# Kernel optimization log

Measured on AMD Instinct MI355X. Metric: run time of the kernel, lower is better.

The kernel has to match this reference:

```python
import jax, jax.numpy as jnp
import numpy as np

D_MODEL = 256
G_CH = 512
N_HEADS = 8
EPS = 1e-6


def setup_inputs() -> dict:
    key0 = jax.random.key(0)
    ks = jax.random.split(key0, 24)
    B, N1, C, G = 2, 65536, D_MODEL, G_CH
    p = 0.05
    inp = {
        'query': jax.random.normal(ks[0], (B, N1, G), jnp.float32),
        'key': jax.random.normal(ks[1], (B, N1, C), jnp.float32),
        'value': jax.random.normal(ks[2], (B, N1, C), jnp.float32),
        # Mheads1: Linear(guidance_channels, d_model, bias=False); stored as [in,out]
        'mheads1_w': jax.random.normal(ks[3], (G, C), jnp.float32) * p,
        # CrossAttentionLayer q/k/v: Linear(d_model, d_model)
        'q_w': jax.random.normal(ks[4], (C, C), jnp.float32) * p,
        'q_b': jax.random.normal(ks[5], (C,), jnp.float32) * p,
        'k_w': jax.random.normal(ks[6], (C, C), jnp.float32) * p,
        'k_b': jax.random.normal(ks[7], (C,), jnp.float32) * p,
        'v_w': jax.random.normal(ks[8], (C, C), jnp.float32) * p,
        'v_b': jax.random.normal(ks[9], (C,), jnp.float32) * p,
        # MSCW local_attn: Linear->ReLU->Linear
        'l1_w': jax.random.normal(ks[10], (C, C), jnp.float32) * p,
        'l1_b': jax.random.normal(ks[11], (C,), jnp.float32) * p,
        'l2_w': jax.random.normal(ks[12], (C, C), jnp.float32) * p,
        'l2_b': jax.random.normal(ks[13], (C,), jnp.float32) * p,
        # MSCW global_attn: Linear->ReLU->Linear
        'g1_w': jax.random.normal(ks[14], (C, C), jnp.float32) * p,
        'g1_b': jax.random.normal(ks[15], (C,), jnp.float32) * p,
        'g2_w': jax.random.normal(ks[16], (C, C), jnp.float32) * p,
        'g2_b': jax.random.normal(ks[17], (C,), jnp.float32) * p,
    }
    return inp


def _haar_pool(feat):
    # feat: [B, C, H, W]; standard WCT2 WavePool: depthwise 2x2 stride-2 Haar conv.
    B, C, H, W = feat.shape
    x = feat.reshape(B, C, H // 2, 2, W // 2, 2)
    a = x[:, :, :, 0, :, 0]
    b = x[:, :, :, 0, :, 1]
    c = x[:, :, :, 1, :, 0]
    d = x[:, :, :, 1, :, 1]
    # Haar: L=[1,1]/sqrt2, Hf=[-1,1]/sqrt2 -> outer-product 2x2 filters, /2 overall
    LL = (a + b + c + d) * 0.5
    LH = (-a + b - c + d) * 0.5
    HL = (-a - b + c + d) * 0.5
    HH = (a - b - c + d) * 0.5
    return LL, LH, HL, HH


def reference(query, key, value, mheads1_w, q_w, q_b, k_w, k_b, v_w, v_b,
              l1_w, l1_b, l2_w, l2_b, g1_w, g1_b, g2_w, g2_b):
    B, n1, C = value.shape
    hw = int(round(n1 ** 0.5))
    q_guid = query @ mheads1_w  # [B, L, C]

    feat = jnp.transpose(key, (0, 2, 1)).reshape(B, C, hw, hw)
    LL, LH, HL, HH = _haar_pool(feat)
    high = HL + LH + HH  # [B, C, hw/2, hw/2]
    low = LL
    high = jnp.transpose(high.reshape(B, C, -1), (0, 2, 1))  # [B, S, C]
    low = jnp.transpose(low.reshape(B, C, -1), (0, 2, 1))

    # MSCW gating
    s = high + low
    pool = jnp.mean(s, axis=1, keepdims=True)
    local = jax.nn.relu(s @ l1_w + l1_b) @ l2_w + l2_b
    glob = jax.nn.relu(pool @ g1_w + g1_b) @ g2_w + g2_b
    wei = jax.nn.sigmoid(local + glob)
    fre = wei * high + low  # [B, S, C]

    # CrossAttentionLayer with linear (elu-feature) attention
    H, Dh = N_HEADS, C // N_HEADS
    qh = (q_guid @ q_w + q_b).reshape(B, -1, H, Dh)
    kh = (fre @ k_w + k_b).reshape(B, -1, H, Dh)
    vh = (fre @ v_w + v_b).reshape(B, -1, H, Dh)
    Q = jax.nn.elu(qh) + 1.0
    K = jax.nn.elu(kh) + 1.0
    S = vh.shape[1]
    Vn = vh / S
    KV = jnp.einsum('nshd,nshv->nhdv', K, Vn)  # [B, H, D, D]
    Z = 1.0 / (jnp.einsum('nlhd,nhd->nlh', Q, K.sum(axis=1)) + EPS)
    out = jnp.einsum('nlhd,nhdv,nlh->nlhv', Q, KV, Z) * S
    return out.reshape(B, -1, C)
```

## Files before the change

kernel.cpp:

```cpp
#include <hip/hip_runtime.h>
#include <math.h>

#define BB 2
#define N1 65536
#define N2 16384
#define CC 256
#define GG 512
#define NH 8
#define DH 32

#define WS_PPART 0
#define WS_GLOB  66048
#define WS_KVP   66560
#define WS_KSP   590848
#define WS_KVT   607232
#define WS_WFP   619520
#define WS_L1T   685056
#define WS_L2T   717824
#define WS_KWT   750592
#define WS_VWT   783360

typedef __attribute__((ext_vector_type(8))) short short8v;
typedef __attribute__((ext_vector_type(4))) float f32x4;

__device__ __forceinline__ ushort f2bf(float x) {
    union { float f; unsigned int u; } v; v.f = x;
    unsigned int u = v.u;
    unsigned int r = (u + 0x7fffu + ((u >> 16) & 1u)) >> 16;
    return (ushort)r;
}

__device__ __forceinline__ float bf2f(ushort x) {
    union { float f; unsigned int u; } v;
    v.u = ((unsigned int)x) << 16;
    return v.f;
}

__device__ __forceinline__ unsigned int cvtpk(float lo, float hi) {
    unsigned int d;
    asm("v_cvt_pk_bf16_f32 %0, %1, %2" : "=v"(d) : "v"(lo), "v"(hi));
    return d;
}

__device__ __forceinline__ void gload16(const void* g, void* l) {
    __builtin_amdgcn_global_load_lds(
        (const __attribute__((address_space(1))) unsigned int*)g,
        (__attribute__((address_space(3))) unsigned int*)l, 16, 0, 0);
}

__global__ __launch_bounds__(256) void k_prep(const float* __restrict__ l1w, const float* __restrict__ l2w,
                                              const float* __restrict__ kw, const float* __restrict__ vw,
                                              const float* __restrict__ mh, const float* __restrict__ qw,
                                              const float* __restrict__ key,
                                              ushort* __restrict__ t0, ushort* __restrict__ t1,
                                              ushort* __restrict__ t2, ushort* __restrict__ t3,
                                              ushort* __restrict__ wfp, float* __restrict__ ppart) {
    int blk = blockIdx.x, t = threadIdx.x;
    if (blk < 1024) {
        int mat = blk >> 8, k = blk & 255, n = t;
        const float* w = mat == 0 ? l1w : mat == 1 ? l2w : mat == 2 ? kw : vw;
        ushort* o = mat == 0 ? t0 : mat == 1 ? t1 : mat == 2 ? t2 : t3;
        o[(((size_t)(n >> 7) * 8 + (k >> 5)) * 128 + (n & 127)) * 32 + (k & 31)] = f2bf(w[k * 256 + n]);
    } else if (blk < 1536) {
        __shared__ float mr[256];
        int g = blk - 1024;
        mr[t] = mh[g * 256 + t];
        __syncthreads();
        float acc = 0.f;
        for (int k = 0; k < 256; k++) acc += mr[k] * qw[k * 256 + t];
        wfp[(((size_t)(g >> 5) * 256 + t) * 32 + (g & 31))] = f2bf(acc);
    } else {
        int p = blk - 1536;
        int b = p >> 7, ci = p & 127;
        float acc = 0.f;
        for (int q = 0; q < 128; q++) {
            size_t idx = ((size_t)b * 65536 + (size_t)(2 * ci + 1) * 256 + (2 * q + 1)) * 256 + t;
            acc += key[idx];
        }
        ppart[(size_t)p * 256 + t] = acc;
    }
}

__global__ __launch_bounds__(256) void k_glob2(const float* __restrict__ ppart,
                                               const float* __restrict__ g1w,
                                               const float* __restrict__ g1b,
                                               const float* __restrict__ g2w,
                                               const float* __restrict__ g2b,
                                               float* __restrict__ glob) {
    __shared__ float pl[256], hid[256];
    int t = threadIdx.x;
    for (int b = 0; b < BB; b++) {
        float s = 0.f;
        for (int p = 0; p < 128; p++) s += ppart[((size_t)b * 128 + p) * 256 + t];
        pl[t] = s * (2.f / 16384.f);
        __syncthreads();
        float acc = g1b[t];
        for (int k = 0; k < 256; k++) acc += pl[k] * g1w[k * 256 + t];
        hid[t] = fmaxf(acc, 0.f);
        __syncthreads();
        float a2 = g2b[t];
        for (int k = 0; k < 256; k++) a2 += hid[k] * g2w[k * 256 + t];
        glob[b * 256 + t] = a2;
        __syncthreads();
    }
}

template <int AMODE, int EPI>
__global__ __launch_bounds__(256) void gemm_bf(const void* __restrict__ Asrc_,
                                               const ushort* __restrict__ Wt,
                                               const float* __restrict__ bias,
                                               void* __restrict__ Outp,
                                               const float* __restrict__ glob,
                                               const float* __restrict__ key) {
    __shared__ __align__(16) ushort smem[8192];
    ushort* As = smem;
    ushort* Bs = smem + 4096;

    const int tid = threadIdx.x;
    const int lane = tid & 63;
    const int w = tid >> 6;
    const int wrow = w >> 1, wcol = w & 1;
    const int bx = blockIdx.x & 1;
    const int by = blockIdx.x >> 1;
    const int r0 = by * 128, n0 = bx * 128;
    const int l15 = lane & 15, l4 = lane >> 4;

    const int loff = lane * 16;
    char* ldsB0 = (char*)Bs + w * 2048;
    char* ldsB1 = (char*)Bs + w * 2048 + 1024;
    const int rowA0 = w * 32 + (lane >> 2);
    const int kbA = (lane & 3) * 16;
    char* ldsA0 = (char*)As + w * 2048;
    char* ldsA1 = (char*)As + w * 2048 + 1024;
    const int srow = tid >> 1, shalf = tid & 1;
    size_t agbase = 0;
    if constexpr (AMODE == 1) {
        int r = r0 + srow;
        int b = r >> 14, rr = r & 16383;
        int ii = rr >> 7, jj = rr & 127;
        agbase = ((size_t)b * 65536 + (size_t)(2 * ii + 1) * 256 + (2 * jj + 1)) * 256 + shalf * 16;
    }

    f32x4 acc[4][4];
#pragma unroll
    for (int i = 0; i < 4; i++)
#pragma unroll
        for (int j = 0; j < 4; j++) acc[i][j] = (f32x4){0.f, 0.f, 0.f, 0.f};

    for (int ks = 0; ks < 8; ks++) {
        const char* btile = (const char*)Wt + (size_t)(bx * 8 + ks) * 8192;
        gload16(btile + w * 2048 + loff, ldsB0);
        gload16(btile + w * 2048 + 1024 + loff, ldsB1);
        if constexpr (AMODE == 0) {
            const char* ab = (const char*)Asrc_;
            gload16(ab + (size_t)(r0 + rowA0) * 512 + ks * 64 + kbA, ldsA0);
            gload16(ab + (size_t)(r0 + rowA0 + 16) * 512 + ks * 64 + kbA, ldsA1);
        } else {
            const float* kf = (const float*)Asrc_;
            float4 f0 = *(const float4*)(kf + agbase + (size_t)ks * 32);
            float4 f1 = *(const float4*)(kf + agbase + (size_t)ks * 32 + 4);
            float4 f2 = *(const float4*)(kf + agbase + (size_t)ks * 32 + 8);
            float4 f3 = *(const float4*)(kf + agbase + (size_t)ks * 32 + 12);
            uint4 lo = {cvtpk(f0.x * 2.f, f0.y * 2.f), cvtpk(f0.z * 2.f, f0.w * 2.f),
                        cvtpk(f1.x * 2.f, f1.y * 2.f), cvtpk(f1.z * 2.f, f1.w * 2.f)};
            uint4 hi = {cvtpk(f2.x * 2.f, f2.y * 2.f), cvtpk(f2.z * 2.f, f2.w * 2.f),
                        cvtpk(f3.x * 2.f, f3.y * 2.f), cvtpk(f3.z * 2.f, f3.w * 2.f)};
            *(uint4*)((char*)As + srow * 64 + shalf * 32) = lo;
            *(uint4*)((char*)As + srow * 64 + shalf * 32 + 16) = hi;
        }
        __syncthreads();

        short8v a[4], bfr[4];
#pragma unroll
        for (int m = 0; m < 4; m++)
            a[m] = *(const short8v*)((const char*)As + (wrow * 64 + m * 16 + l15) * 64 + l4 * 16);
#pragma unroll
        for (int n = 0; n < 4; n++)
            bfr[n] = *(const short8v*)((const char*)Bs + (wcol * 64 + n * 16 + l15) * 64 + l4 * 16);
#pragma unroll
        for (int m = 0; m < 4; m++)
#pragma unroll
            for (int n = 0; n < 4; n++)
                acc[m][n] = __builtin_amdgcn_mfma_f32_16x16x32_bf16(a[m], bfr[n], acc[m][n], 0, 0, 0);
        __syncthreads();
    }

    const int b = r0 >> 14;
    float bv[4], gv[4];
#pragma unroll
    for (int n = 0; n < 4; n++) {
        int c = n0 + wcol * 64 + n * 16 + l15;
        bv[n] = bias[c];
        if constexpr (EPI == 1) gv[n] = glob[b * 256 + c];
    }
#pragma unroll
    for (int m = 0; m < 4; m++) {
#pragma unroll
        for (int n = 0; n < 4; n++) {
            int c = n0 + wcol * 64 + n * 16 + l15;
#pragma unroll
            for (int r = 0; r < 4; r++) {
                int row = wrow * 64 + m * 16 + l4 * 4 + r;
                int R = r0 + row;
                float x = acc[m][n][r] + bv[n];
                if constexpr (EPI == 0) {
                    ((ushort*)Outp)[(size_t)R * 256 + c] = f2bf(fmaxf(x, 0.f));
                } else if constexpr (EPI == 1) {
                    int rr = R & 16383;
                    int ii = rr >> 7, jj = rr & 127;
                    size_t kb = ((size_t)b * 65536 + (size_t)(2 * ii) * 256 + 2 * jj) * 256 + c;
                    float ka = key[kb];
                    float kb2 = key[kb + 256];
                    float kc2 = key[kb + 65536];
                    float kd2 = key[kb + 65536 + 256];
                    float low = 0.5f * (ka + kb2 + kc2 + kd2);
                    float high = 0.5f * (3.f * kd2 - ka - kb2 - kc2);
                    float wei = 1.f / (1.f + __expf(-(x + gv[n])));
                    ((ushort*)Outp)[(size_t)R * 256 + c] = f2bf(wei * high + low);
                } else if constexpr (EPI == 4) {
                    ((ushort*)Outp)[(size_t)R * 256 + c] = f2bf((x > 0.f) ? x + 1.f : __expf(x));
                } else {
                    ((ushort*)Outp)[(size_t)R * 256 + c] = f2bf(x);
                }
            }
        }
    }
}

__global__ __launch_bounds__(256) void k_kv_part(const ushort* __restrict__ Km,
                                                 const ushort* __restrict__ Vn,
                                                 float* __restrict__ kvp,
                                                 float* __restrict__ ksp) {
    __shared__ float Kl[8][33];
    __shared__ float Vl[8][33];
    int t = threadIdx.x;
    int c = blockIdx.x & 31, h = (blockIdx.x >> 5) & 7, b = blockIdx.x >> 8;
    int d = t >> 3, vq = (t & 7) * 4;
    int lr = t >> 5, lc = t & 31;
    float acc0 = 0, acc1 = 0, acc2 = 0, acc3 = 0, ks = 0;
    size_t rowbase = (size_t)b * 16384 + (size_t)c * 512;
    for (int s0 = 0; s0 < 512; s0 += 8) {
        size_t idx = (rowbase + s0 + lr) * 256 + h * 32 + lc;
        Kl[lr][lc] = bf2f(Km[idx]);
        Vl[lr][lc] = bf2f(Vn[idx]);
        __syncthreads();
#pragma unroll
        for (int rr = 0; rr < 8; rr++) {
            float kd = Kl[rr][d];
            acc0 += kd * Vl[rr][vq];
            acc1 += kd * Vl[rr][vq + 1];
            acc2 += kd * Vl[rr][vq + 2];
            acc3 += kd * Vl[rr][vq + 3];
            ks += kd;
        }
        __syncthreads();
    }
    size_t ob = ((size_t)(b * 8 + h) * 32 + c) * 1024 + d * 32 + vq;
    kvp[ob] = acc0; kvp[ob + 1] = acc1; kvp[ob + 2] = acc2; kvp[ob + 3] = acc3;
    if ((t & 7) == 0) ksp[((b * 8 + h) * 32 + c) * 32 + d] = ks;
}

__global__ __launch_bounds__(256) void k_kv_reduce(const float* __restrict__ kvp,
                                                   const float* __restrict__ ksp,
                                                   ushort* __restrict__ kvt) {
    int bh = blockIdx.x, t = threadIdx.x;
    for (int e = t; e < 1024; e += 256) {
        float s = 0.f;
        for (int cc = 0; cc < 32; cc++) s += kvp[((size_t)bh * 32 + cc) * 1024 + e];
        int d = e >> 5, v = e & 31;
        kvt[((size_t)bh * 48 + v) * 32 + d] = f2bf(s);
    }
    if (t < 32) {
        float s = 0.f;
        for (int cc = 0; cc < 32; cc++) s += ksp[(bh * 32 + cc) * 32 + t];
        kvt[((size_t)bh * 48 + 32) * 32 + t] = f2bf(s);
    }
    for (int z = t; z < 480; z += 256) kvt[(size_t)bh * 48 * 32 + 33 * 32 + z] = 0;
}

__global__ __launch_bounds__(512, 4) void k_qattn_mfma(const float* __restrict__ query,
                                                       const ushort* __restrict__ wfp,
                                                       const float* __restrict__ qb,
                                                       const ushort* __restrict__ kvt,
                                                       float* __restrict__ Out) {
    __shared__ __align__(16) ushort smem[32768];
    ushort* As = smem;
    ushort* Bs = smem + 4096;

    const int tid = threadIdx.x;
    const int lane = tid & 63;
    const int wid = tid >> 6;
    const int wrow = wid >> 2, wcol = wid & 3;
    const int by = blockIdx.x;
    const int r0 = by * 128;
    const int l15 = lane & 15, l4 = lane >> 4;

    const int loff = lane * 16;
    char* ldsB0 = (char*)Bs + wid * 2048;
    char* ldsB1 = (char*)Bs + wid * 2048 + 1024;

    const int srow = tid >> 2;
    const int skq = tid & 3;
    const size_t agbase = (size_t)(r0 + srow) * 512 + skq * 8;

    f32x4 acc[4][4];
#pragma unroll
    for (int i = 0; i < 4; i++)
#pragma unroll
        for (int j = 0; j < 4; j++) acc[i][j] = (f32x4){0.f, 0.f, 0.f, 0.f};

    for (int ks = 0; ks < 16; ks++) {
        const char* btile = (const char*)wfp + (size_t)ks * 16384;
        gload16(btile + wid * 2048 + loff, ldsB0);
        gload16(btile + wid * 2048 + 1024 + loff, ldsB1);
        {
            float4 f0 = *(const float4*)(query + agbase + (size_t)ks * 32);
            float4 f1 = *(const float4*)(query + agbase + (size_t)ks * 32 + 4);
            uint4 pk = {cvtpk(f0.x, f0.y), cvtpk(f0.z, f0.w),
                        cvtpk(f1.x, f1.y), cvtpk(f1.z, f1.w)};
            *(uint4*)((char*)As + srow * 64 + skq * 16) = pk;
        }
        __syncthreads();

        short8v a[4], bfr[4];
#pragma unroll
        for (int m = 0; m < 4; m++)
            a[m] = *(const short8v*)((const char*)As + (wrow * 64 + m * 16 + l15) * 64 + l4 * 16);
#pragma unroll
        for (int n = 0; n < 4; n++)
            bfr[n] = *(const short8v*)((const char*)Bs + (wcol * 64 + n * 16 + l15) * 64 + l4 * 16);
#pragma unroll
        for (int m = 0; m < 4; m++)
#pragma unroll
            for (int n = 0; n < 4; n++)
                acc[m][n] = __builtin_amdgcn_mfma_f32_16x16x32_bf16(a[m], bfr[n], acc[m][n], 0, 0, 0);
        __syncthreads();
    }

    float qbv[4];
#pragma unroll
    for (int n = 0; n < 4; n++) qbv[n] = qb[wcol * 64 + n * 16 + l15];
#pragma unroll
    for (int m = 0; m < 4; m++) {
#pragma unroll
        for (int n = 0; n < 4; n++) {
#pragma unroll
            for (int r = 0; r < 4; r++) {
                int rl = m * 16 + l4 * 4 + r;
                int cl = n * 16 + l15;
                float x = acc[m][n][r] + qbv[n];
                float q = x > 0.f ? x + 1.f : __expf(x);
                int byte = wid * 8192 + ((rl * 128 + cl * 2) ^ ((rl & 7) << 4));
                *(ushort*)((char*)smem + byte) = f2bf(q);
            }
        }
    }
    __syncthreads();

    const int bb = r0 >> 16;
#pragma unroll
    for (int hi = 0; hi < 2; hi++) {
        int h = wcol * 2 + hi;
        int bh = bb * 8 + h;
        const ushort* kb = kvt + (size_t)bh * 48 * 32;
        short8v bk0 = *(const short8v*)(kb + (0 * 16 + l15) * 32 + l4 * 8);
        short8v bk1 = *(const short8v*)(kb + (1 * 16 + l15) * 32 + l4 * 8);
        short8v bkz = *(const short8v*)(kb + (2 * 16 + l15) * 32 + l4 * 8);
#pragma unroll
        for (int m = 0; m < 4; m++) {
            int rl = m * 16 + l15;
            int byte = wid * 8192 + ((rl * 128 + hi * 64 + l4 * 16) ^ ((rl & 7) << 4));
            short8v aq = *(const short8v*)((const char*)smem + byte);
            f32x4 zero = (f32x4){0.f, 0.f, 0.f, 0.f};
            f32x4 o0 = __builtin_amdgcn_mfma_f32_16x16x32_bf16(aq, bk0, zero, 0, 0, 0);
            f32x4 o1 = __builtin_amdgcn_mfma_f32_16x16x32_bf16(aq, bk1, zero, 0, 0, 0);
            f32x4 oz = __builtin_amdgcn_mfma_f32_16x16x32_bf16(aq, bkz, zero, 0, 0, 0);
#pragma unroll
            for (int r = 0; r < 4; r++) {
                float z = __shfl(oz[r], (lane & 48));
                float sc = 1.f / (z + 1e-6f);
                int grow = r0 + wrow * 64 + m * 16 + l4 * 4 + r;
                int gcol = wcol * 64 + hi * 32 + l15;
                Out[(size_t)grow * 256 + gcol] = o0[r] * sc;
                Out[(size_t)grow * 256 + gcol + 16] = o1[r] * sc;
            }
        }
    }
}

extern "C" void kernel_launch(void* const* d_in, const int* in_sizes, int n_in,
                              void* d_out, int out_size, void* d_ws, size_t ws_size,
                              hipStream_t stream) {
    const float* query = (const float*)d_in[0];
    const float* key = (const float*)d_in[1];
    const float* mh = (const float*)d_in[3];
    const float* q_w = (const float*)d_in[4];
    const float* q_b = (const float*)d_in[5];
    const float* k_w = (const float*)d_in[6];
    const float* k_b = (const float*)d_in[7];
    const float* v_w = (const float*)d_in[8];
    const float* v_b = (const float*)d_in[9];
    const float* l1_w = (const float*)d_in[10];
    const float* l1_b = (const float*)d_in[11];
    const float* l2_w = (const float*)d_in[12];
    const float* l2_b = (const float*)d_in[13];
    const float* g1_w = (const float*)d_in[14];
    const float* g1_b = (const float*)d_in[15];
    const float* g2_w = (const float*)d_in[16];
    const float* g2_b = (const float*)d_in[17];

    float* out = (float*)d_out;
    float* ws = (float*)d_ws;

    float* ppart = ws + WS_PPART;
    float* glob = ws + WS_GLOB;
    float* kvp = ws + WS_KVP;
    float* ksp = ws + WS_KSP;
    ushort* kvt = (ushort*)(ws + WS_KVT);
    ushort* wfp = (ushort*)(ws + WS_WFP);
    ushort* l1t = (ushort*)(ws + WS_L1T);
    ushort* l2t = (ushort*)(ws + WS_L2T);
    ushort* kwt = (ushort*)(ws + WS_KWT);
    ushort* vwt = (ushort*)(ws + WS_VWT);

    ushort* t = (ushort*)out;
    ushort* fre = (ushort*)(out + 4194304);
    ushort* Km = (ushort*)(out + 8388608);
    ushort* Vn = (ushort*)(out + 12582912);

    k_prep<<<1792, 256, 0, stream>>>(l1_w, l2_w, k_w, v_w, mh, q_w, key,
                                     l1t, l2t, kwt, vwt, wfp, ppart);
    k_glob2<<<1, 256, 0, stream>>>(ppart, g1_w, g1_b, g2_w, g2_b, glob);

    gemm_bf<1, 0><<<512, 256, 0, stream>>>(key, l1t, l1_b, t, nullptr, nullptr);
    gemm_bf<0, 1><<<512, 256, 0, stream>>>(t, l2t, l2_b, fre, glob, key);
    gemm_bf<0, 4><<<512, 256, 0, stream>>>(fre, kwt, k_b, Km, nullptr, nullptr);
    gemm_bf<0, 5><<<512, 256, 0, stream>>>(fre, vwt, v_b, Vn, nullptr, nullptr);

    k_kv_part<<<512, 256, 0, stream>>>(Km, Vn, kvp, ksp);
    k_kv_reduce<<<16, 256, 0, stream>>>(kvp, ksp, kvt);

    k_qattn_mfma<<<1024, 512, 0, stream>>>(query, wfp, q_b, kvt, out);
}
```

Measured before the change: 271.6 us.

## Fuse four chained MSCW/K/V GEMMs into one kernel keeping tiles in LDS

```diff
diff --git a/kernel.cpp b/kernel.cpp
--- a/kernel.cpp
+++ b/kernel.cpp
@@ -2,12 +2,6 @@
 #include <math.h>
 
 #define BB 2
-#define N1 65536
-#define N2 16384
-#define CC 256
-#define GG 512
-#define NH 8
-#define DH 32
 
 #define WS_PPART 0
 #define WS_GLOB  66048
@@ -60,7 +54,7 @@
         int mat = blk >> 8, k = blk & 255, n = t;
         const float* w = mat == 0 ? l1w : mat == 1 ? l2w : mat == 2 ? kw : vw;
         ushort* o = mat == 0 ? t0 : mat == 1 ? t1 : mat == 2 ? t2 : t3;
-        o[(((size_t)(n >> 7) * 8 + (k >> 5)) * 128 + (n & 127)) * 32 + (k & 31)] = f2bf(w[k * 256 + n]);
+        o[(size_t)(k >> 5) * 8192 + (size_t)((k >> 3) & 3) * 2048 + n * 8 + (k & 7)] = f2bf(w[k * 256 + n]);
     } else if (blk < 1536) {
         __shared__ float mr[256];
         int g = blk - 1024;
@@ -68,7 +62,7 @@
         __syncthreads();
         float acc = 0.f;
         for (int k = 0; k < 256; k++) acc += mr[k] * qw[k * 256 + t];
-        wfp[(((size_t)(g >> 5) * 256 + t) * 32 + (g & 31))] = f2bf(acc);
+        wfp[(size_t)(g >> 3) * 2048 + t * 8 + (g & 7)] = f2bf(acc);
     } else {
         int p = blk - 1536;
         int b = p >> 7, ci = p & 127;
@@ -105,123 +99,235 @@
     }
 }
 
-template <int AMODE, int EPI>
-__global__ __launch_bounds__(256) void gemm_bf(const void* __restrict__ Asrc_,
-                                               const ushort* __restrict__ Wt,
-                                               const float* __restrict__ bias,
-                                               void* __restrict__ Outp,
-                                               const float* __restrict__ glob,
-                                               const float* __restrict__ key) {
-    __shared__ __align__(16) ushort smem[8192];
-    ushort* As = smem;
-    ushort* Bs = smem + 4096;
+__global__ __launch_bounds__(256, 3) void k_mid(const float* __restrict__ key,
+                                                const ushort* __restrict__ l1t,
+                                                const ushort* __restrict__ l2t,
+                                                const ushort* __restrict__ kwt,
+                                                const ushort* __restrict__ vwt,
+                                                const float* __restrict__ l1b,
+                                                const float* __restrict__ l2b,
+                                                const float* __restrict__ kbias,
+                                                const float* __restrict__ vbias,
+                                                const float* __restrict__ glob,
+                                                ushort* __restrict__ Km,
+                                                ushort* __restrict__ Vn) {
+    __shared__ __align__(16) ushort smem[26624];
+    ushort* tile = smem;
+    ushort* As = smem + 16384;
+    ushort* Bs = smem + 18432;
 
     const int tid = threadIdx.x;
     const int lane = tid & 63;
-    const int w = tid >> 6;
-    const int wrow = w >> 1, wcol = w & 1;
-    const int bx = blockIdx.x & 1;
-    const int by = blockIdx.x >> 1;
-    const int r0 = by * 128, n0 = bx * 128;
+    const int wid = tid >> 6;
+    const int wrow = wid >> 1, wcol = wid & 1;
+    const int R0 = blockIdx.x * 64;
+    const int b = R0 >> 14;
     const int l15 = lane & 15, l4 = lane >> 4;
 
-    const int loff = lane * 16;
-    char* ldsB0 = (char*)Bs + w * 2048;
-    char* ldsB1 = (char*)Bs + w * 2048 + 1024;
-    const int rowA0 = w * 32 + (lane >> 2);
-    const int kbA = (lane & 3) * 16;
-    char* ldsA0 = (char*)As + w * 2048;
-    char* ldsA1 = (char*)As + w * 2048 + 1024;
-    const int srow = tid >> 1, shalf = tid & 1;
-    size_t agbase = 0;
-    if constexpr (AMODE == 1) {
-        int r = r0 + srow;
-        int b = r >> 14, rr = r & 16383;
+    const int srow = tid & 63, skq = tid >> 6;
+    size_t agbase;
+    {
+        int R = R0 + srow;
+        int rr = R & 16383;
         int ii = rr >> 7, jj = rr & 127;
-        agbase = ((size_t)b * 65536 + (size_t)(2 * ii + 1) * 256 + (2 * jj + 1)) * 256 + shalf * 16;
-    }
-
-    f32x4 acc[4][4];
-#pragma unroll
-    for (int i = 0; i < 4; i++)
-#pragma unroll
-        for (int j = 0; j < 4; j++) acc[i][j] = (f32x4){0.f, 0.f, 0.f, 0.f};
+        agbase = ((size_t)b * 65536 + (size_t)(2 * ii + 1) * 256 + (2 * jj + 1)) * 256 + skq * 8;
+    }
+
+    f32x4 acc[2][8];
+
+#pragma unroll
+    for (int m = 0; m < 2; m++)
+#pragma unroll
+        for (int n = 0; n < 8; n++) acc[m][n] = (f32x4){0.f, 0.f, 0.f, 0.f};
 
     for (int ks = 0; ks < 8; ks++) {
-        const char* btile = (const char*)Wt + (size_t)(bx * 8 + ks) * 8192;
-        gload16(btile + w * 2048 + loff, ldsB0);
-        gload16(btile + w * 2048 + 1024 + loff, ldsB1);
-        if constexpr (AMODE == 0) {
-            const char* ab = (const char*)Asrc_;
-            gload16(ab + (size_t)(r0 + rowA0) * 512 + ks * 64 + kbA, ldsA0);
-            gload16(ab + (size_t)(r0 + rowA0 + 16) * 512 + ks * 64 + kbA, ldsA1);
-        } else {
-            const float* kf = (const float*)Asrc_;
-            float4 f0 = *(const float4*)(kf + agbase + (size_t)ks * 32);
-            float4 f1 = *(const float4*)(kf + agbase + (size_t)ks * 32 + 4);
-            float4 f2 = *(const float4*)(kf + agbase + (size_t)ks * 32 + 8);
-            float4 f3 = *(const float4*)(kf + agbase + (size_t)ks * 32 + 12);
-            uint4 lo = {cvtpk(f0.x * 2.f, f0.y * 2.f), cvtpk(f0.z * 2.f, f0.w * 2.f),
-                        cvtpk(f1.x * 2.f, f1.y * 2.f), cvtpk(f1.z * 2.f, f1.w * 2.f)};
-            uint4 hi = {cvtpk(f2.x * 2.f, f2.y * 2.f), cvtpk(f2.z * 2.f, f2.w * 2.f),
-                        cvtpk(f3.x * 2.f, f3.y * 2.f), cvtpk(f3.z * 2.f, f3.w * 2.f)};
-            *(uint4*)((char*)As + srow * 64 + shalf * 32) = lo;
-            *(uint4*)((char*)As + srow * 64 + shalf * 32 + 16) = hi;
-        }
-        __syncthreads();
-
-        short8v a[4], bfr[4];
-#pragma unroll
-        for (int m = 0; m < 4; m++)
-            a[m] = *(const short8v*)((const char*)As + (wrow * 64 + m * 16 + l15) * 64 + l4 * 16);
-#pragma unroll
-        for (int n = 0; n < 4; n++)
-            bfr[n] = *(const short8v*)((const char*)Bs + (wcol * 64 + n * 16 + l15) * 64 + l4 * 16);
-#pragma unroll
-        for (int m = 0; m < 4; m++)
-#pragma unroll
-            for (int n = 0; n < 4; n++)
-                acc[m][n] = __builtin_amdgcn_mfma_f32_16x16x32_bf16(a[m], bfr[n], acc[m][n], 0, 0, 0);
-        __syncthreads();
-    }
-
-    const int b = r0 >> 14;
-    float bv[4], gv[4];
-#pragma unroll
-    for (int n = 0; n < 4; n++) {
-        int c = n0 + wcol * 64 + n * 16 + l15;
-        bv[n] = bias[c];
-        if constexpr (EPI == 1) gv[n] = glob[b * 256 + c];
-    }
-#pragma unroll
-    for (int m = 0; m < 4; m++) {
-#pragma unroll
-        for (int n = 0; n < 4; n++) {
-            int c = n0 + wcol * 64 + n * 16 + l15;
+        float4 f0 = *(const float4*)(key + agbase + (size_t)ks * 32);
+        float4 f1 = *(const float4*)(key + agbase + (size_t)ks * 32 + 4);
+        uint4 pk = {cvtpk(f0.x * 2.f, f0.y * 2.f), cvtpk(f0.z * 2.f, f0.w * 2.f),
+                    cvtpk(f1.x * 2.f, f1.y * 2.f), cvtpk(f1.z * 2.f, f1.w * 2.f)};
+        *(uint4*)((char*)As + skq * 1024 + srow * 16) = pk;
+        {
+            const char* pan = (const char*)l1t + (size_t)ks * 16384;
+            char* dst = (char*)Bs + wid * 4096;
+#pragma unroll
+            for (int i = 0; i < 4; i++)
+                gload16(pan + wid * 4096 + i * 1024 + lane * 16, dst + i * 1024);
+        }
+        __syncthreads();
+        short8v a[2], bf[8];
+#pragma unroll
+        for (int m = 0; m < 2; m++)
+            a[m] = *(const short8v*)((const char*)As + l4 * 1024 + (wrow * 32 + m * 16 + l15) * 16);
+#pragma unroll
+        for (int n = 0; n < 8; n++)
+            bf[n] = *(const short8v*)((const char*)Bs + l4 * 4096 + (wcol * 128 + n * 16 + l15) * 16);
+#pragma unroll
+        for (int m = 0; m < 2; m++)
+#pragma unroll
+            for (int n = 0; n < 8; n++)
+                acc[m][n] = __builtin_amdgcn_mfma_f32_16x16x32_bf16(a[m], bf[n], acc[m][n], 0, 0, 0);
+        __syncthreads();
+    }
+#pragma unroll
+    for (int m = 0; m < 2; m++) {
+#pragma unroll
+        for (int n = 0; n < 8; n++) {
+            int col = wcol * 128 + n * 16 + l15;
+            float bias = l1b[col];
 #pragma unroll
             for (int r = 0; r < 4; r++) {
-                int row = wrow * 64 + m * 16 + l4 * 4 + r;
-                int R = r0 + row;
-                float x = acc[m][n][r] + bv[n];
-                if constexpr (EPI == 0) {
-                    ((ushort*)Outp)[(size_t)R * 256 + c] = f2bf(fmaxf(x, 0.f));
-                } else if constexpr (EPI == 1) {
-                    int rr = R & 16383;
-                    int ii = rr >> 7, jj = rr & 127;
-                    size_t kb = ((size_t)b * 65536 + (size_t)(2 * ii) * 256 + 2 * jj) * 256 + c;
-                    float ka = key[kb];
-                    float kb2 = key[kb + 256];
-                    float kc2 = key[kb + 65536];
-                    float kd2 = key[kb + 65536 + 256];
-                    float low = 0.5f * (ka + kb2 + kc2 + kd2);
-                    float high = 0.5f * (3.f * kd2 - ka - kb2 - kc2);
-                    float wei = 1.f / (1.f + __expf(-(x + gv[n])));
-                    ((ushort*)Outp)[(size_t)R * 256 + c] = f2bf(wei * high + low);
-                } else if constexpr (EPI == 4) {
-                    ((ushort*)Outp)[(size_t)R * 256 + c] = f2bf((x > 0.f) ? x + 1.f : __expf(x));
-                } else {
-                    ((ushort*)Outp)[(size_t)R * 256 + c] = f2bf(x);
-                }
+                int row = wrow * 32 + m * 16 + l4 * 4 + r;
+                float x = acc[m][n][r] + bias;
+                int byte = (row * 512 + col * 2) ^ ((row & 7) << 4);
+                *(ushort*)((char*)tile + byte) = f2bf(fmaxf(x, 0.f));
+            }
+        }
+    }
+
+#pragma unroll
+    for (int m = 0; m < 2; m++)
+#pragma unroll
+        for (int n = 0; n < 8; n++) acc[m][n] = (f32x4){0.f, 0.f, 0.f, 0.f};
+
+    for (int ks = 0; ks < 8; ks++) {
+        {
+            const char* pan = (const char*)l2t + (size_t)ks * 16384;
+            char* dst = (char*)Bs + wid * 4096;
+#pragma unroll
+            for (int i = 0; i < 4; i++)
+                gload16(pan + wid * 4096 + i * 1024 + lane * 16, dst + i * 1024);
+        }
+        __syncthreads();
+        short8v a[2], bf[8];
+#pragma unroll
+        for (int m = 0; m < 2; m++) {
+            int row = wrow * 32 + m * 16 + l15;
+            int byte = (row * 512 + ks * 64 + l4 * 16) ^ ((row & 7) << 4);
+            a[m] = *(const short8v*)((const char*)tile + byte);
+        }
+#pragma unroll
+        for (int n = 0; n < 8; n++)
+            bf[n] = *(const short8v*)((const char*)Bs + l4 * 4096 + (wcol * 128 + n * 16 + l15) * 16);
+#pragma unroll
+        for (int m = 0; m < 2; m++)
+#pragma unroll
+            for (int n = 0; n < 8; n++)
+                acc[m][n] = __builtin_amdgcn_mfma_f32_16x16x32_bf16(a[m], bf[n], acc[m][n], 0, 0, 0);
+        __syncthreads();
+    }
+#pragma unroll
+    for (int m = 0; m < 2; m++) {
+#pragma unroll
+        for (int n = 0; n < 8; n++) {
+            int col = wcol * 128 + n * 16 + l15;
+            float bias = l2b[col] + glob[b * 256 + col];
+#pragma unroll
+            for (int r = 0; r < 4; r++) {
+                int row = wrow * 32 + m * 16 + l4 * 4 + r;
+                int rr = (R0 + row) & 16383;
+                int ii = rr >> 7, jj = rr & 127;
+                size_t kb = ((size_t)b * 65536 + (size_t)(2 * ii) * 256 + 2 * jj) * 256 + col;
+                float ka = key[kb];
+                float kb2 = key[kb + 256];
+                float kc2 = key[kb + 65536];
+                float kd2 = key[kb + 65536 + 256];
+                float low = 0.5f * (ka + kb2 + kc2 + kd2);
+                float high = 0.5f * (3.f * kd2 - ka - kb2 - kc2);
+                float x = acc[m][n][r] + bias;
+                float wei = 1.f / (1.f + __expf(-x));
+                int byte = (row * 512 + col * 2) ^ ((row & 7) << 4);
+                *(ushort*)((char*)tile + byte) = f2bf(wei * high + low);
+            }
+        }
+    }
+
+#pragma unroll
+    for (int m = 0; m < 2; m++)
+#pragma unroll
+        for (int n = 0; n < 8; n++) acc[m][n] = (f32x4){0.f, 0.f, 0.f, 0.f};
+
+    for (int ks = 0; ks < 8; ks++) {
+        {
+            const char* pan = (const char*)kwt + (size_t)ks * 16384;
+            char* dst = (char*)Bs + wid * 4096;
+#pragma unroll
+            for (int i = 0; i < 4; i++)
+                gload16(pan + wid * 4096 + i * 1024 + lane * 16, dst + i * 1024);
+        }
+        __syncthreads();
+        short8v a[2], bf[8];
+#pragma unroll
+        for (int m = 0; m < 2; m++) {
+            int row = wrow * 32 + m * 16 + l15;
+            int byte = (row * 512 + ks * 64 + l4 * 16) ^ ((row & 7) << 4);
+            a[m] = *(const short8v*)((const char*)tile + byte);
+        }
+#pragma unroll
+        for (int n = 0; n < 8; n++)
+            bf[n] = *(const short8v*)((const char*)Bs + l4 * 4096 + (wcol * 128 + n * 16 + l15) * 16);
+#pragma unroll
+        for (int m = 0; m < 2; m++)
+#pragma unroll
+            for (int n = 0; n < 8; n++)
+                acc[m][n] = __builtin_amdgcn_mfma_f32_16x16x32_bf16(a[m], bf[n], acc[m][n], 0, 0, 0);
+        __syncthreads();
+    }
+#pragma unroll
+    for (int m = 0; m < 2; m++) {
+#pragma unroll
+        for (int n = 0; n < 8; n++) {
+            int col = wcol * 128 + n * 16 + l15;
+            float bias = kbias[col];
+#pragma unroll
+            for (int r = 0; r < 4; r++) {
+                int row = wrow * 32 + m * 16 + l4 * 4 + r;
+                float x = acc[m][n][r] + bias;
+                Km[(size_t)(R0 + row) * 256 + col] = f2bf((x > 0.f) ? x + 1.f : __expf(x));
+            }
+        }
+    }
+
+#pragma unroll
+    for (int m = 0; m < 2; m++)
+#pragma unroll
+        for (int n = 0; n < 8; n++) acc[m][n] = (f32x4){0.f, 0.f, 0.f, 0.f};
+
+    for (int ks = 0; ks < 8; ks++) {
+        {
+            const char* pan = (const char*)vwt + (size_t)ks * 16384;
+            char* dst = (char*)Bs + wid * 4096;
+#pragma unroll
+            for (int i = 0; i < 4; i++)
+                gload16(pan + wid * 4096 + i * 1024 + lane * 16, dst + i * 1024);
+        }
+        __syncthreads();
+        short8v a[2], bf[8];
+#pragma unroll
+        for (int m = 0; m < 2; m++) {
+            int row = wrow * 32 + m * 16 + l15;
+            int byte = (row * 512 + ks * 64 + l4 * 16) ^ ((row & 7) << 4);
+            a[m] = *(const short8v*)((const char*)tile + byte);
+        }
+#pragma unroll
+        for (int n = 0; n < 8; n++)
+            bf[n] = *(const short8v*)((const char*)Bs + l4 * 4096 + (wcol * 128 + n * 16 + l15) * 16);
+#pragma unroll
+        for (int m = 0; m < 2; m++)
+#pragma unroll
+            for (int n = 0; n < 8; n++)
+                acc[m][n] = __builtin_amdgcn_mfma_f32_16x16x32_bf16(a[m], bf[n], acc[m][n], 0, 0, 0);
+        __syncthreads();
+    }
+#pragma unroll
+    for (int m = 0; m < 2; m++) {
+#pragma unroll
+        for (int n = 0; n < 8; n++) {
+            int col = wcol * 128 + n * 16 + l15;
+            float bias = vbias[col];
+#pragma unroll
+            for (int r = 0; r < 4; r++) {
+                int row = wrow * 32 + m * 16 + l4 * 4 + r;
+                Vn[(size_t)(R0 + row) * 256 + col] = f2bf(acc[m][n][r] + bias);
             }
         }
     }
@@ -285,23 +391,18 @@
                                                        float* __restrict__ Out) {
     __shared__ __align__(16) ushort smem[32768];
     ushort* As = smem;
-    ushort* Bs = smem + 4096;
+    ushort* Bs = smem + 8192;
 
     const int tid = threadIdx.x;
     const int lane = tid & 63;
     const int wid = tid >> 6;
     const int wrow = wid >> 2, wcol = wid & 3;
-    const int by = blockIdx.x;
-    const int r0 = by * 128;
+    const int R0 = blockIdx.x * 128;
     const int l15 = lane & 15, l4 = lane >> 4;
 
-    const int loff = lane * 16;
-    char* ldsB0 = (char*)Bs + wid * 2048;
-    char* ldsB1 = (char*)Bs + wid * 2048 + 1024;
-
-    const int srow = tid >> 2;
-    const int skq = tid & 3;
-    const size_t agbase = (size_t)(r0 + srow) * 512 + skq * 8;
+    const int srow = tid & 127;
+    const int khalf = tid >> 7;
+    const size_t agbase = (size_t)(R0 + srow) * 512 + khalf * 16;
 
     f32x4 acc[4][4];
 #pragma unroll
@@ -309,31 +410,41 @@
 #pragma unroll
         for (int j = 0; j < 4; j++) acc[i][j] = (f32x4){0.f, 0.f, 0.f, 0.f};
 
-    for (int ks = 0; ks < 16; ks++) {
-        const char* btile = (const char*)wfp + (size_t)ks * 16384;
-        gload16(btile + wid * 2048 + loff, ldsB0);
-        gload16(btile + wid * 2048 + 1024 + loff, ldsB1);
+    for (int ks = 0; ks < 8; ks++) {
         {
-            float4 f0 = *(const float4*)(query + agbase + (size_t)ks * 32);
-            float4 f1 = *(const float4*)(query + agbase + (size_t)ks * 32 + 4);
-            uint4 pk = {cvtpk(f0.x, f0.y), cvtpk(f0.z, f0.w),
-                        cvtpk(f1.x, f1.y), cvtpk(f1.z, f1.w)};
-            *(uint4*)((char*)As + srow * 64 + skq * 16) = pk;
-        }
-        __syncthreads();
-
-        short8v a[4], bfr[4];
-#pragma unroll
-        for (int m = 0; m < 4; m++)
-            a[m] = *(const short8v*)((const char*)As + (wrow * 64 + m * 16 + l15) * 64 + l4 * 16);
-#pragma unroll
-        for (int n = 0; n < 4; n++)
-            bfr[n] = *(const short8v*)((const char*)Bs + (wcol * 64 + n * 16 + l15) * 64 + l4 * 16);
-#pragma unroll
-        for (int m = 0; m < 4; m++)
+            const float* qp = query + agbase + (size_t)ks * 64;
+            float4 f0 = *(const float4*)(qp);
+            float4 f1 = *(const float4*)(qp + 4);
+            float4 f2 = *(const float4*)(qp + 8);
+            float4 f3 = *(const float4*)(qp + 12);
+            uint4 lo = {cvtpk(f0.x, f0.y), cvtpk(f0.z, f0.w), cvtpk(f1.x, f1.y), cvtpk(f1.z, f1.w)};
+            uint4 hi = {cvtpk(f2.x, f2.y), cvtpk(f2.z, f2.w), cvtpk(f3.x, f3.y), cvtpk(f3.z, f3.w)};
+            *(uint4*)((char*)As + (khalf * 2) * 2048 + srow * 16) = lo;
+            *(uint4*)((char*)As + (khalf * 2 + 1) * 2048 + srow * 16) = hi;
+        }
+        {
+            const char* pan = (const char*)wfp + (size_t)ks * 32768;
+#pragma unroll
+            for (int i = 0; i < 4; i++)
+                gload16(pan + i * 8192 + wid * 1024 + lane * 16, (char*)Bs + i * 8192 + wid * 1024);
+        }
+        __syncthreads();
+
+#pragma unroll
+        for (int sub = 0; sub < 2; sub++) {
+            short8v a[4], bf[4];
+#pragma unroll
+            for (int m = 0; m < 4; m++)
+                a[m] = *(const short8v*)((const char*)As + (sub * 4 + l4) * 2048 + (wrow * 64 + m * 16 + l15) * 16);
 #pragma unroll
             for (int n = 0; n < 4; n++)
-                acc[m][n] = __builtin_amdgcn_mfma_f32_16x16x32_bf16(a[m], bfr[n], acc[m][n], 0, 0, 0);
+                bf[n] = *(const short8v*)((const char*)Bs + (sub * 4 + l4) * 4096 + (wcol * 64 + n * 16 + l15) * 16);
+#pragma unroll
+            for (int m = 0; m < 4; m++)
+#pragma unroll
+                for (int n = 0; n < 4; n++)
+                    acc[m][n] = __builtin_amdgcn_mfma_f32_16x16x32_bf16(a[m], bf[n], acc[m][n], 0, 0, 0);
+        }
         __syncthreads();
     }
 
@@ -357,7 +468,7 @@
     }
     __syncthreads();
 
-    const int bb = r0 >> 16;
+    const int bb = R0 >> 16;
 #pragma unroll
     for (int hi = 0; hi < 2; hi++) {
         int h = wcol * 2 + hi;
@@ -379,7 +490,7 @@
             for (int r = 0; r < 4; r++) {
                 float z = __shfl(oz[r], (lane & 48));
                 float sc = 1.f / (z + 1e-6f);
-                int grow = r0 + wrow * 64 + m * 16 + l4 * 4 + r;
+                int grow = R0 + wrow * 64 + m * 16 + l4 * 4 + r;
                 int gcol = wcol * 64 + hi * 32 + l15;
                 Out[(size_t)grow * 256 + gcol] = o0[r] * sc;
                 Out[(size_t)grow * 256 + gcol + 16] = o1[r] * sc;
@@ -423,19 +534,15 @@
     ushort* kwt = (ushort*)(ws + WS_KWT);
     ushort* vwt = (ushort*)(ws + WS_VWT);
 
-    ushort* t = (ushort*)out;
-    ushort* fre = (ushort*)(out + 4194304);
-    ushort* Km = (ushort*)(out + 8388608);
-    ushort* Vn = (ushort*)(out + 12582912);
+    ushort* Km = (ushort*)out;
+    ushort* Vn = (ushort*)(out + 4194304);
 
     k_prep<<<1792, 256, 0, stream>>>(l1_w, l2_w, k_w, v_w, mh, q_w, key,
                                      l1t, l2t, kwt, vwt, wfp, ppart);
     k_glob2<<<1, 256, 0, stream>>>(ppart, g1_w, g1_b, g2_w, g2_b, glob);
 
-    gemm_bf<1, 0><<<512, 256, 0, stream>>>(key, l1t, l1_b, t, nullptr, nullptr);
-    gemm_bf<0, 1><<<512, 256, 0, stream>>>(t, l2t, l2_b, fre, glob, key);
-    gemm_bf<0, 4><<<512, 256, 0, stream>>>(fre, kwt, k_b, Km, nullptr, nullptr);
-    gemm_bf<0, 5><<<512, 256, 0, stream>>>(fre, vwt, v_b, Vn, nullptr, nullptr);
+    k_mid<<<512, 256, 0, stream>>>(key, l1t, l2t, kwt, vwt,
+                                   l1_b, l2_b, k_b, v_b, glob, Km, Vn);
 
     k_kv_part<<<512, 256, 0, stream>>>(Km, Vn, kvp, ksp);
     k_kv_reduce<<<16, 256, 0, stream>>>(kvp, ksp, kvt);
```

New measurement: 277.6 us. 2.2% more time.

## Retile query-attention kernel to 64-row blocks with 256 threads

Applied to the files above, without the earlier changes.

```diff
diff --git a/kernel.cpp b/kernel.cpp
--- a/kernel.cpp
+++ b/kernel.cpp
@@ -2,12 +2,6 @@
 #include <math.h>
 
 #define BB 2
-#define N1 65536
-#define N2 16384
-#define CC 256
-#define GG 512
-#define NH 8
-#define DH 32
 
 #define WS_PPART 0
 #define WS_GLOB  66048
@@ -278,30 +272,24 @@
     for (int z = t; z < 480; z += 256) kvt[(size_t)bh * 48 * 32 + 33 * 32 + z] = 0;
 }
 
-__global__ __launch_bounds__(512, 4) void k_qattn_mfma(const float* __restrict__ query,
+__global__ __launch_bounds__(256, 4) void k_qattn_mfma(const float* __restrict__ query,
                                                        const ushort* __restrict__ wfp,
                                                        const float* __restrict__ qb,
                                                        const ushort* __restrict__ kvt,
                                                        float* __restrict__ Out) {
-    __shared__ __align__(16) ushort smem[32768];
+    __shared__ __align__(16) ushort smem[16384];
     ushort* As = smem;
-    ushort* Bs = smem + 4096;
+    ushort* Bs = smem + 2048;
 
     const int tid = threadIdx.x;
     const int lane = tid & 63;
     const int wid = tid >> 6;
-    const int wrow = wid >> 2, wcol = wid & 3;
-    const int by = blockIdx.x;
-    const int r0 = by * 128;
+    const int R0 = blockIdx.x * 64;
     const int l15 = lane & 15, l4 = lane >> 4;
 
-    const int loff = lane * 16;
-    char* ldsB0 = (char*)Bs + wid * 2048;
-    char* ldsB1 = (char*)Bs + wid * 2048 + 1024;
-
-    const int srow = tid >> 2;
-    const int skq = tid & 3;
-    const size_t agbase = (size_t)(r0 + srow) * 512 + skq * 8;
+    const int srow = tid & 63;
+    const int skq = tid >> 6;
+    const size_t agbase = (size_t)(R0 + srow) * 512 + skq * 8;
 
     f32x4 acc[4][4];
 #pragma unroll
@@ -310,9 +298,6 @@
         for (int j = 0; j < 4; j++) acc[i][j] = (f32x4){0.f, 0.f, 0.f, 0.f};
 
     for (int ks = 0; ks < 16; ks++) {
-        const char* btile = (const char*)wfp + (size_t)ks * 16384;
-        gload16(btile + wid * 2048 + loff, ldsB0);
-        gload16(btile + wid * 2048 + 1024 + loff, ldsB1);
         {
             float4 f0 = *(const float4*)(query + agbase + (size_t)ks * 32);
             float4 f1 = *(const float4*)(query + agbase + (size_t)ks * 32 + 4);
@@ -320,15 +305,22 @@
                         cvtpk(f1.x, f1.y), cvtpk(f1.z, f1.w)};
             *(uint4*)((char*)As + srow * 64 + skq * 16) = pk;
         }
+        {
+            const char* pan = (const char*)wfp + (size_t)ks * 16384;
+#pragma unroll
+            for (int i = 0; i < 4; i++)
+                gload16(pan + wid * 4096 + i * 1024 + lane * 16,
+                        (char*)Bs + wid * 4096 + i * 1024);
+        }
         __syncthreads();
 
         short8v a[4], bfr[4];
 #pragma unroll
         for (int m = 0; m < 4; m++)
-            a[m] = *(const short8v*)((const char*)As + (wrow * 64 + m * 16 + l15) * 64 + l4 * 16);
+            a[m] = *(const short8v*)((const char*)As + (m * 16 + l15) * 64 + l4 * 16);
 #pragma unroll
         for (int n = 0; n < 4; n++)
-            bfr[n] = *(const short8v*)((const char*)Bs + (wcol * 64 + n * 16 + l15) * 64 + l4 * 16);
+            bfr[n] = *(const short8v*)((const char*)Bs + (wid * 64 + n * 16 + l15) * 64 + l4 * 16);
 #pragma unroll
         for (int m = 0; m < 4; m++)
 #pragma unroll
@@ -339,28 +331,28 @@
 
     float qbv[4];
 #pragma unroll
-    for (int n = 0; n < 4; n++) qbv[n] = qb[wcol * 64 + n * 16 + l15];
+    for (int n = 0; n < 4; n++) qbv[n] = qb[wid * 64 + n * 16 + l15];
 #pragma unroll
     for (int m = 0; m < 4; m++) {
 #pragma unroll
         for (int n = 0; n < 4; n++) {
 #pragma unroll
             for (int r = 0; r < 4; r++) {
-                int rl = m * 16 + l4 * 4 + r;
-                int cl = n * 16 + l15;
+                int row = m * 16 + l4 * 4 + r;
+                int col = wid * 64 + n * 16 + l15;
                 float x = acc[m][n][r] + qbv[n];
                 float q = x > 0.f ? x + 1.f : __expf(x);
-                int byte = wid * 8192 + ((rl * 128 + cl * 2) ^ ((rl & 7) << 4));
+                int byte = (row * 512 + col * 2) ^ ((row & 7) << 4);
                 *(ushort*)((char*)smem + byte) = f2bf(q);
             }
         }
     }
     __syncthreads();
 
-    const int bb = r0 >> 16;
+    const int bb = R0 >> 14 >> 2;
 #pragma unroll
     for (int hi = 0; hi < 2; hi++) {
-        int h = wcol * 2 + hi;
+        int h = wid * 2 + hi;
         int bh = bb * 8 + h;
         const ushort* kb = kvt + (size_t)bh * 48 * 32;
         short8v bk0 = *(const short8v*)(kb + (0 * 16 + l15) * 32 + l4 * 8);
@@ -368,8 +360,8 @@
         short8v bkz = *(const short8v*)(kb + (2 * 16 + l15) * 32 + l4 * 8);
 #pragma unroll
         for (int m = 0; m < 4; m++) {
-            int rl = m * 16 + l15;
-            int byte = wid * 8192 + ((rl * 128 + hi * 64 + l4 * 16) ^ ((rl & 7) << 4));
+            int row = m * 16 + l15;
+            int byte = (row * 512 + h * 64 + l4 * 16) ^ ((row & 7) << 4);
             short8v aq = *(const short8v*)((const char*)smem + byte);
             f32x4 zero = (f32x4){0.f, 0.f, 0.f, 0.f};
             f32x4 o0 = __builtin_amdgcn_mfma_f32_16x16x32_bf16(aq, bk0, zero, 0, 0, 0);
@@ -379,8 +371,8 @@
             for (int r = 0; r < 4; r++) {
                 float z = __shfl(oz[r], (lane & 48));
                 float sc = 1.f / (z + 1e-6f);
-                int grow = r0 + wrow * 64 + m * 16 + l4 * 4 + r;
-                int gcol = wcol * 64 + hi * 32 + l15;
+                int grow = R0 + m * 16 + l4 * 4 + r;
+                int gcol = h * 32 + l15;
                 Out[(size_t)grow * 256 + gcol] = o0[r] * sc;
                 Out[(size_t)grow * 256 + gcol + 16] = o1[r] * sc;
             }
@@ -440,5 +432,5 @@
     k_kv_part<<<512, 256, 0, stream>>>(Km, Vn, kvp, ksp);
     k_kv_reduce<<<16, 256, 0, stream>>>(kvp, ksp, kvt);
 
-    k_qattn_mfma<<<1024, 512, 0, stream>>>(query, wfp, q_b, kvt, out);
-}
+    k_qattn_mfma<<<2048, 256, 0, stream>>>(query, wfp, q_b, kvt, out);
+}
```

Measured after the change: 289.7 us. 1.07x slower.

## Double-buffer query GEMM tiles with direct fp32 global-to-LDS loads

Applied to the files above, without the earlier changes.

```diff
diff --git a/kernel.cpp b/kernel.cpp
--- a/kernel.cpp
+++ b/kernel.cpp
@@ -2,12 +2,6 @@
 #include <math.h>
 
 #define BB 2
-#define N1 65536
-#define N2 16384
-#define CC 256
-#define GG 512
-#define NH 8
-#define DH 32
 
 #define WS_PPART 0
 #define WS_GLOB  66048
@@ -283,25 +277,24 @@
                                                        const float* __restrict__ qb,
                                                        const ushort* __restrict__ kvt,
                                                        float* __restrict__ Out) {
-    __shared__ __align__(16) ushort smem[32768];
-    ushort* As = smem;
-    ushort* Bs = smem + 4096;
+    __shared__ __align__(16) char smem[65536];
+    char* As0 = smem;
+    char* As1 = smem + 16384;
+    char* Bs0 = smem + 32768;
+    char* Bs1 = smem + 49152;
 
     const int tid = threadIdx.x;
     const int lane = tid & 63;
     const int wid = tid >> 6;
     const int wrow = wid >> 2, wcol = wid & 3;
-    const int by = blockIdx.x;
-    const int r0 = by * 128;
+    const int R0 = blockIdx.x * 128;
     const int l15 = lane & 15, l4 = lane >> 4;
 
-    const int loff = lane * 16;
-    char* ldsB0 = (char*)Bs + wid * 2048;
-    char* ldsB1 = (char*)Bs + wid * 2048 + 1024;
-
-    const int srow = tid >> 2;
-    const int skq = tid & 3;
-    const size_t agbase = (size_t)(r0 + srow) * 512 + skq * 8;
+    const int arow0 = wid * 16 + (lane >> 3);
+    const int achunk = (lane & 7) ^ (lane >> 3);
+    const float* aga = query + (size_t)(R0 + arow0) * 512 + achunk * 4;
+    const int wb = wid * 2048;
+    const int bglo = wb + lane * 16;
 
     f32x4 acc[4][4];
 #pragma unroll
@@ -309,33 +302,56 @@
 #pragma unroll
         for (int j = 0; j < 4; j++) acc[i][j] = (f32x4){0.f, 0.f, 0.f, 0.f};
 
+#define QSTAGE(dA, dB, kss)                                                     \
+    do {                                                                        \
+        const float* ga_ = aga + (size_t)(kss) * 32;                            \
+        gload16(ga_, (dA) + wb);                                                \
+        gload16(ga_ + 8 * 512, (dA) + wb + 1024);                               \
+        const char* pan_ = (const char*)wfp + (size_t)(kss) * 16384 + bglo;     \
+        gload16(pan_, (dB) + wb);                                               \
+        gload16(pan_ + 1024, (dB) + wb + 1024);                                 \
+    } while (0)
+
+    QSTAGE(As0, Bs0, 0);
+    asm volatile("s_waitcnt vmcnt(0)" ::: "memory");
+    __builtin_amdgcn_s_barrier();
+    __builtin_amdgcn_sched_barrier(0);
+
     for (int ks = 0; ks < 16; ks++) {
-        const char* btile = (const char*)wfp + (size_t)ks * 16384;
-        gload16(btile + wid * 2048 + loff, ldsB0);
-        gload16(btile + wid * 2048 + 1024 + loff, ldsB1);
-        {
-            float4 f0 = *(const float4*)(query + agbase + (size_t)ks * 32);
-            float4 f1 = *(const float4*)(query + agbase + (size_t)ks * 32 + 4);
-            uint4 pk = {cvtpk(f0.x, f0.y), cvtpk(f0.z, f0.w),
-                        cvtpk(f1.x, f1.y), cvtpk(f1.z, f1.w)};
-            *(uint4*)((char*)As + srow * 64 + skq * 16) = pk;
-        }
-        __syncthreads();
-
-        short8v a[4], bfr[4];
-#pragma unroll
-        for (int m = 0; m < 4; m++)
-            a[m] = *(const short8v*)((const char*)As + (wrow * 64 + m * 16 + l15) * 64 + l4 * 16);
+        const char* bA = (ks & 1) ? As1 : As0;
+        const char* bB = (ks & 1) ? Bs1 : Bs0;
+        char* nA = (ks & 1) ? As0 : As1;
+        char* nB = (ks & 1) ? Bs0 : Bs1;
+        if (ks < 15) QSTAGE(nA, nB, ks + 1);
+
+        short8v bfr[4];
 #pragma unroll
         for (int n = 0; n < 4; n++)
-            bfr[n] = *(const short8v*)((const char*)Bs + (wcol * 64 + n * 16 + l15) * 64 + l4 * 16);
-#pragma unroll
-        for (int m = 0; m < 4; m++)
+            bfr[n] = *(const short8v*)(bB + (wcol * 64 + n * 16 + l15) * 64 + l4 * 16);
+#pragma unroll
+        for (int m = 0; m < 4; m++) {
+            int row = wrow * 64 + m * 16 + l15;
+            int j0 = (l4 * 2) ^ (l15 & 7);
+            const char* rp = bA + row * 128;
+            f32x4 lo = *(const f32x4*)(rp + j0 * 16);
+            f32x4 hi = *(const f32x4*)(rp + (j0 ^ 1) * 16);
+            union { uint4 u; short8v s; } av;
+            av.u = (uint4){cvtpk(lo.x, lo.y), cvtpk(lo.z, lo.w),
+                           cvtpk(hi.x, hi.y), cvtpk(hi.z, hi.w)};
 #pragma unroll
             for (int n = 0; n < 4; n++)
-                acc[m][n] = __builtin_amdgcn_mfma_f32_16x16x32_bf16(a[m], bfr[n], acc[m][n], 0, 0, 0);
-        __syncthreads();
-    }
+                acc[m][n] = __builtin_amdgcn_mfma_f32_16x16x32_bf16(av.s, bfr[n], acc[m][n], 0, 0, 0);
+        }
+
+        if (ks < 15) {
+            asm volatile("s_waitcnt vmcnt(0)" ::: "memory");
+            __builtin_amdgcn_s_barrier();
+            __builtin_amdgcn_sched_barrier(0);
+        }
+    }
+#undef QSTAGE
+
+    __syncthreads();
 
     float qbv[4];
 #pragma unroll
@@ -351,13 +367,13 @@
                 float x = acc[m][n][r] + qbv[n];
                 float q = x > 0.f ? x + 1.f : __expf(x);
                 int byte = wid * 8192 + ((rl * 128 + cl * 2) ^ ((rl & 7) << 4));
-                *(ushort*)((char*)smem + byte) = f2bf(q);
+                *(ushort*)(smem + byte) = f2bf(q);
             }
         }
     }
     __syncthreads();
 
-    const int bb = r0 >> 16;
+    const int bb = R0 >> 16;
 #pragma unroll
     for (int hi = 0; hi < 2; hi++) {
         int h = wcol * 2 + hi;
@@ -370,7 +386,7 @@
         for (int m = 0; m < 4; m++) {
             int rl = m * 16 + l15;
             int byte = wid * 8192 + ((rl * 128 + hi * 64 + l4 * 16) ^ ((rl & 7) << 4));
-            short8v aq = *(const short8v*)((const char*)smem + byte);
+            short8v aq = *(const short8v*)(smem + byte);
             f32x4 zero = (f32x4){0.f, 0.f, 0.f, 0.f};
             f32x4 o0 = __builtin_amdgcn_mfma_f32_16x16x32_bf16(aq, bk0, zero, 0, 0, 0);
             f32x4 o1 = __builtin_amdgcn_mfma_f32_16x16x32_bf16(aq, bk1, zero, 0, 0, 0);
@@ -379,7 +395,7 @@
             for (int r = 0; r < 4; r++) {
                 float z = __shfl(oz[r], (lane & 48));
                 float sc = 1.f / (z + 1e-6f);
-                int grow = r0 + wrow * 64 + m * 16 + l4 * 4 + r;
+                int grow = R0 + wrow * 64 + m * 16 + l4 * 4 + r;
                 int gcol = wcol * 64 + hi * 32 + l15;
                 Out[(size_t)grow * 256 + gcol] = o0[r] * sc;
                 Out[(size_t)grow * 256 + gcol + 16] = o1[r] * sc;
```

New measurement: 265.6 us. -2.2%, faster.
